# Kernel optimization log

Measured on AMD Instinct MI355X. Metric: run time of the kernel, lower is better.

## Reference

```python
import jax, jax.numpy as jnp
import numpy as np

H = 16  # number of heads

def setup_inputs() -> dict:
    key = jax.random.key(0)
    ks = jax.random.split(key, 8)
    B, T, D = 4, 2048, 1024
    s = 0.02
    return {
        "query": jax.random.normal(ks[0], (B, T, D), jnp.float32),
        "key":   jax.random.normal(ks[1], (B, T, D), jnp.float32),
        "value": jax.random.normal(ks[2], (B, T, D), jnp.float32),
        "mask":  jnp.ones((B, T, T), jnp.int32),
        # torch nn.Linear weights: [out_features, in_features]
        "Wq": jax.random.normal(ks[3], (D, D), jnp.float32) * s,
        "Wk": jax.random.normal(ks[4], (D, D), jnp.float32) * s,
        "Wv": jax.random.normal(ks[5], (D, D), jnp.float32) * s,
        "Wo": jax.random.normal(ks[6], (D, D), jnp.float32) * s,
        "bo": jnp.zeros((D,), jnp.float32),
    }

def reference(query, key, value, mask, Wq, Wk, Wv, Wo, bo):
    B, Tq, _ = query.shape
    Tk = key.shape[1]
    Dv = Wv.shape[0]
    # linear projections (y = x @ W^T), split into heads: [B, H, T, dh]
    Q = jnp.einsum('btd,ed->bte', query, Wq).reshape(B, Tq, H, -1).transpose(0, 2, 1, 3)
    K = jnp.einsum('btd,ed->bte', key,   Wk).reshape(B, Tk, H, -1).transpose(0, 2, 1, 3)
    V = jnp.einsum('btd,ed->bte', value, Wv).reshape(B, Tk, H, -1).transpose(0, 2, 1, 3)
    d_k = K.shape[-1]
    scores = jnp.einsum('bhqd,bhkd->bhqk', Q, K) / jnp.sqrt(jnp.asarray(d_k, Q.dtype))
    # mask broadcast: [B,1,Tq,Tk]; masked_fill(mask==0, -1e9)
    scores = jnp.where(mask[:, None] == 0, jnp.asarray(-1e9, scores.dtype), scores)
    attn = jax.nn.softmax(scores, axis=-1)
    Z = jnp.einsum('bhqk,bhkd->bhqd', attn, V)          # [B,H,Tq,dh]
    Zc = Z.transpose(0, 2, 1, 3).reshape(B, Tq, Dv)     # concat heads
    return jnp.einsum('btd,ed->bte', Zc, Wo) + bo
```

## Files before the change

kernel.cpp:

```cpp
#include <hip/hip_runtime.h>

typedef __bf16 bf16x8 __attribute__((ext_vector_type(8)));
typedef __bf16 bf16x4 __attribute__((ext_vector_type(4)));
typedef float f32x4 __attribute__((ext_vector_type(4)));
typedef unsigned short u16;
typedef unsigned long long u64;

#define NX 8388608
#define NW 1048576

__device__ __forceinline__ u16 f2bf(float f) {
  union { float f; unsigned u; } c; c.f = f;
  unsigned u = c.u;
  u += 0x7fffu + ((u >> 16) & 1u);
  return (u16)(u >> 16);
}

__device__ __forceinline__ f32x4 mfma16(bf16x8 a, bf16x8 b, f32x4 c) {
  return __builtin_amdgcn_mfma_f32_16x16x32_bf16(a, b, c, 0, 0, 0);
}

__device__ __forceinline__ void gld16(void* lds, const void* g) {
  __builtin_amdgcn_global_load_lds(
      (const __attribute__((address_space(1))) unsigned int*)g,
      (__attribute__((address_space(3))) unsigned int*)lds, 16, 0, 0);
}

__global__ __launch_bounds__(256) void cast_all(
    const float* __restrict__ q, const float* __restrict__ k,
    const float* __restrict__ v, const float* __restrict__ wq,
    const float* __restrict__ wk, const float* __restrict__ wv,
    const float* __restrict__ wo, u16* __restrict__ xbf, u16* __restrict__ wbf,
    const int* __restrict__ mask, u64* __restrict__ bits) {
  if (blockIdx.x >= 14336) {
    const int row = (blockIdx.x - 14336) * 4 + (threadIdx.x >> 6);
    const int lane = threadIdx.x & 63;
    const int* mrow = mask + (long long)row * 2048;
#pragma unroll
    for (int it = 0; it < 32; it++) {
      u64 w = __ballot(mrow[it * 64 + lane] != 0);
      if (lane == 0) bits[row * 32 + it] = w;
    }
    return;
  }
  long long i = ((long long)blockIdx.x * 256 + threadIdx.x) * 8;
  const float* src; u16* dst; long long off;
  if (i < (long long)NX)            { src = q; dst = xbf;            off = i; }
  else if (i < 2LL * NX)            { src = k; dst = xbf + NX;       off = i - NX; }
  else if (i < 3LL * NX)            { src = v; dst = xbf + 2LL * NX; off = i - 2LL * NX; }
  else {
    long long j = i - 3LL * NX;
    int w = (int)(j / NW); off = j - (long long)w * NW;
    src = (w == 0) ? wq : (w == 1) ? wk : (w == 2) ? wv : wo;
    dst = wbf + (long long)w * NW;
  }
  float4 a = *(const float4*)(src + off);
  float4 b = *(const float4*)(src + off + 4);
  u16 o[8] = {f2bf(a.x), f2bf(a.y), f2bf(a.z), f2bf(a.w),
              f2bf(b.x), f2bf(b.y), f2bf(b.z), f2bf(b.w)};
  *(uint4*)(dst + off) = *(const uint4*)o;
}

template <int MODE>
__global__ __launch_bounds__(256, 4) void gemm128(
    const u16* __restrict__ Abase, const u16* __restrict__ Wbase,
    u16* __restrict__ oq, u16* __restrict__ ok, u16* __restrict__ ovt,
    const float* __restrict__ bias, float* __restrict__ of) {
  __shared__ alignas(16) u16 smem[2][128 * 64];
  u16* sA = smem[0];
  u16* sB = smem[1];
  const u16* A = Abase;
  const u16* W = Wbase;
  if (MODE == 0) { A += (long long)blockIdx.z * NX; W += (long long)blockIdx.z * NW; }
  const int tid = threadIdx.x, wave = tid >> 6, lane = tid & 63;
  const int quad = lane >> 4, l15 = lane & 15;
  const int id = blockIdx.y * 8 + blockIdx.x;
  const int id2 = (id & 7) * 64 + (id >> 3);
  const int m0 = (id2 >> 3) * 128, n0 = (id2 & 7) * 128;
  const int wm = (wave & 1) * 64, wn = (wave >> 1) * 64;
  const int lr = lane >> 3;
  const int gc = (lane & 7) ^ lr;
  f32x4 acc[4][4];
#pragma unroll
  for (int i = 0; i < 4; i++)
#pragma unroll
    for (int j = 0; j < 4; j++) acc[i][j] = (f32x4){0.f, 0.f, 0.f, 0.f};

  for (int ks = 0; ks < 16; ks++) {
    const int k0 = ks * 64;
    __syncthreads();
#pragma unroll
    for (int t = 0; t < 4; t++) {
      const int rb = wave * 32 + t * 8;
      gld16(&sA[rb * 64], &A[(m0 + rb + lr) * 1024 + k0 + gc * 8]);
      gld16(&sB[rb * 64], &W[(n0 + rb + lr) * 1024 + k0 + gc * 8]);
    }
    __syncthreads();
#pragma unroll
    for (int kc = 0; kc < 2; kc++) {
      bf16x8 aF[4], bF[4];
#pragma unroll
      for (int i = 0; i < 4; i++)
        aF[i] = *(const bf16x8*)&sA[(wm + 16 * i + l15) * 64 +
                                    (((kc * 4 + quad) ^ (l15 & 7)) * 8)];
#pragma unroll
      for (int j = 0; j < 4; j++)
        bF[j] = *(const bf16x8*)&sB[(wn + 16 * j + l15) * 64 +
                                    (((kc * 4 + quad) ^ (l15 & 7)) * 8)];
#pragma unroll
      for (int i = 0; i < 4; i++)
#pragma unroll
        for (int j = 0; j < 4; j++) acc[i][j] = mfma16(aF[i], bF[j], acc[i][j]);
    }
  }

  if (MODE == 0) {
    const int z = blockIdx.z;
    __syncthreads();
    if (z < 2) {
      const float qscale = (z == 0) ? 0.18033688f : 1.0f;
      u16* dst = (z == 0) ? oq : ok;
      u16* sT = &smem[0][0] + wave * 4096;
#pragma unroll
      for (int i = 0; i < 4; i++)
#pragma unroll
        for (int j = 0; j < 4; j++)
#pragma unroll
          for (int r = 0; r < 4; r++) {
            int m = 16 * i + quad * 4 + r;
            int d = 16 * j + l15;
            sT[m * 64 + (((d >> 3) ^ (m & 7)) * 8) + (d & 7)] =
                f2bf(acc[i][j][r] * qscale);
          }
      const int bq = m0 >> 11, t0w = (m0 + wm) & 2047;
      const int hq = (n0 + wn) >> 6;
      u16* dq = dst + ((long long)((bq << 4) + hq) * 2048 + t0w + lane) * 64;
#pragma unroll
      for (int c = 0; c < 8; c++) {
        uint4 val = *(const uint4*)&sT[lane * 64 + ((c ^ (lane & 7)) * 8)];
        *(uint4*)(dq + c * 8) = val;
      }
    } else {
      u16* sT = &smem[0][0] + wave * 4096;
#pragma unroll
      for (int i = 0; i < 4; i++)
#pragma unroll
        for (int j = 0; j < 4; j++)
#pragma unroll
          for (int r = 0; r < 4; r++) {
            int m = 16 * i + quad * 4 + r;
            int n = 16 * j + l15;
            sT[n * 64 + (((m >> 3) ^ (n & 7)) * 8) + (m & 7)] = f2bf(acc[i][j][r]);
          }
      const int b = m0 >> 11, t0 = (m0 + wm) & 2047;
      const int h = (n0 + wn) >> 6;
      u16* dst = ovt + ((long long)((b << 4) + h)) * 131072 + lane * 2048 + t0;
#pragma unroll
      for (int c = 0; c < 8; c++) {
        uint4 val = *(const uint4*)&sT[lane * 64 + ((c ^ (lane & 7)) * 8)];
        *(uint4*)(dst + c * 8) = val;
      }
    }
  } else {
    float bb[4];
#pragma unroll
    for (int j = 0; j < 4; j++) bb[j] = bias[n0 + wn + 16 * j + l15];
    __syncthreads();
    float* sW = (float*)&smem[0][0] + wave * 2048;
#pragma unroll
    for (int p = 0; p < 2; p++) {
#pragma unroll
      for (int i = 0; i < 4; i++)
#pragma unroll
        for (int jj = 0; jj < 2; jj++)
#pragma unroll
          for (int r = 0; r < 4; r++) {
            int m = 16 * i + quad * 4 + r;
            int d = 16 * jj + l15;
            sW[m * 32 + (((d >> 2) ^ (m & 7)) * 4) + (d & 3)] =
                acc[i][2 * p + jj][r] + bb[2 * p + jj];
          }
      float* dof = of + (long long)(m0 + wm + lane) * 1024 + n0 + wn + p * 32;
#pragma unroll
      for (int c = 0; c < 8; c++) {
        float4 val = *(const float4*)&sW[lane * 32 + ((c ^ (lane & 7)) * 4)];
        *(float4*)(dof + c * 4) = val;
      }
    }
  }
}

__device__ __forceinline__ void stage_tile(
    u16* sKb, u16* sVb, const u16* __restrict__ Kh, const u16* __restrict__ Vt,
    int bh, int kt, int wave, int lr8, int gc8) {
#pragma unroll
  for (int t = 0; t < 2; t++) {
    const int rb = wave * 16 + t * 8;
    const int c = rb + lr8;
    const int kap = (c & 32) + (((c >> 2) & 3) << 3) + ((c & 16) >> 2) + (c & 3);
    gld16(&sKb[rb * 64], &Kh[(bh * 2048 + kt * 64 + kap) * 64 + gc8 * 8]);
    gld16(&sVb[rb * 64], &Vt[(bh * 64 + rb + lr8) * 2048 + kt * 64 + gc8 * 8]);
  }
}

__global__ __launch_bounds__(256, 4) void attn(
    const u16* __restrict__ Qh, const u16* __restrict__ Kh,
    const u16* __restrict__ Vt, const u64* __restrict__ mbits,
    u16* __restrict__ Zc) {
  __shared__ alignas(16) u16 sK[2][64 * 64];
  __shared__ alignas(16) u16 sV[2][64 * 64];
  const int tid = threadIdx.x, wave = tid >> 6, lane = tid & 63;
  const int quad = lane >> 4, l15 = lane & 15;
  const int id = blockIdx.y * 16 + blockIdx.x;
  const int id2 = (id & 7) * 128 + (id >> 3);
  const int bh = id2 >> 4, qt = id2 & 15;
  const int b = bh >> 4, h = bh & 15;
  const int q0 = qt * 128 + wave * 32;
  const int lr8 = lane >> 3, gc8 = (lane & 7) ^ lr8;

  bf16x8 qa[2][2];
#pragma unroll
  for (int g = 0; g < 2; g++)
#pragma unroll
    for (int kc = 0; kc < 2; kc++)
      qa[g][kc] = *(const bf16x8*)&Qh[(bh * 2048 + q0 + g * 16 + l15) * 64 +
                                      kc * 32 + quad * 8];

  const u64* mrow = mbits + (long long)(b * 2048 + q0) * 32;
  u64 am = ~0ull;
#pragma unroll
  for (int i = 0; i < 16; i++) am &= mrow[lane * 16 + i];
  const bool allfull = __all(am == ~0ull);

  f32x4 oacc[2][4];
#pragma unroll
  for (int g = 0; g < 2; g++)
#pragma unroll
    for (int j = 0; j < 4; j++) oacc[g][j] = (f32x4){0.f, 0.f, 0.f, 0.f};
  float lv[2] = {0.f, 0.f};

  stage_tile(&sK[0][0], &sV[0][0], Kh, Vt, bh, 0, wave, lr8, gc8);
  const f32x4 z4 = (f32x4){0.f, 0.f, 0.f, 0.f};

  for (int kt = 0; kt < 32; kt++) {
    const int cur = kt & 1;
    __syncthreads();
    if (kt < 31)
      stage_tile(&sK[cur ^ 1][0], &sV[cur ^ 1][0], Kh, Vt, bh, kt + 1,
                 wave, lr8, gc8);

    bf16x8 kF[2][4];
#pragma unroll
    for (int kc = 0; kc < 2; kc++)
#pragma unroll
      for (int j = 0; j < 4; j++)
        kF[kc][j] = *(const bf16x8*)&sK[cur][(16 * j + l15) * 64 +
                                            (((kc * 4 + quad) ^ (l15 & 7)) * 8)];
    f32x4 sacc[2][4];
    __builtin_amdgcn_s_setprio(1);
#pragma unroll
    for (int j = 0; j < 4; j++)
#pragma unroll
      for (int g = 0; g < 2; g++) sacc[g][j] = mfma16(kF[0][j], qa[g][0], z4);
#pragma unroll
    for (int j = 0; j < 4; j++)
#pragma unroll
      for (int g = 0; g < 2; g++)
        sacc[g][j] = mfma16(kF[1][j], qa[g][1], sacc[g][j]);
    __builtin_amdgcn_s_setprio(0);

    bf16x8 pa[2][2];
    if (allfull) {
#pragma unroll
      for (int g = 0; g < 2; g++) {
        float ls = 0.f;
#pragma unroll
        for (int kc = 0; kc < 2; kc++) {
          bf16x8 pk;
#pragma unroll
          for (int e = 0; e < 8; e++) {
            float p = __builtin_amdgcn_exp2f(sacc[g][2 * kc + (e >> 2)][e & 3]);
            ls += p;
            pk[e] = (__bf16)p;
          }
          pa[g][kc] = pk;
        }
        lv[g] += ls;
      }
    } else {
#pragma unroll
      for (int g = 0; g < 2; g++) {
        u64 w = mbits[(long long)(b * 2048 + q0 + g * 16 + l15) * 32 + kt];
        float ls = 0.f;
#pragma unroll
        for (int kc = 0; kc < 2; kc++) {
          bf16x8 pk;
#pragma unroll
          for (int e = 0; e < 8; e++) {
            float p = __builtin_amdgcn_exp2f(sacc[g][2 * kc + (e >> 2)][e & 3]);
            p = ((w >> (32 * kc + 8 * quad + e)) & 1ull) ? p : 0.f;
            ls += p;
            pk[e] = (__bf16)p;
          }
          pa[g][kc] = pk;
        }
        lv[g] += ls;
      }
    }

    bf16x8 vF[2][4];
#pragma unroll
    for (int kc = 0; kc < 2; kc++)
#pragma unroll
      for (int j = 0; j < 4; j++)
        vF[kc][j] = *(const bf16x8*)&sV[cur][(16 * j + l15) * 64 +
                                             (((kc * 4 + quad) ^ (l15 & 7)) * 8)];
    __builtin_amdgcn_s_setprio(1);
#pragma unroll
    for (int kc = 0; kc < 2; kc++)
#pragma unroll
      for (int g = 0; g < 2; g++)
#pragma unroll
        for (int j = 0; j < 4; j++)
          oacc[g][j] = mfma16(pa[g][kc], vF[kc][j], oacc[g][j]);
    __builtin_amdgcn_s_setprio(0);
  }

#pragma unroll
  for (int g = 0; g < 2; g++) {
    float s = lv[g];
    s += __shfl_xor(s, 16);
    s += __shfl_xor(s, 32);
    float inv[4];
#pragma unroll
    for (int r = 0; r < 4; r++)
      inv[r] = 1.f / __shfl(s, quad * 4 + r);
#pragma unroll
    for (int j = 0; j < 4; j++)
#pragma unroll
      for (int r = 0; r < 4; r++) {
        int t = q0 + g * 16 + quad * 4 + r;
        Zc[(b * 2048 + t) * 1024 + h * 64 + 16 * j + l15] =
            f2bf(oacc[g][j][r] * inv[r]);
      }
  }
}

extern "C" void kernel_launch(void* const* d_in, const int* in_sizes, int n_in,
                              void* d_out, int out_size, void* d_ws, size_t ws_size,
                              hipStream_t stream) {
  (void)in_sizes; (void)n_in; (void)out_size; (void)ws_size;
  const float* q    = (const float*)d_in[0];
  const float* k    = (const float*)d_in[1];
  const float* v    = (const float*)d_in[2];
  const int*   mask = (const int*)d_in[3];
  const float* Wq   = (const float*)d_in[4];
  const float* Wk   = (const float*)d_in[5];
  const float* Wv   = (const float*)d_in[6];
  const float* Wo   = (const float*)d_in[7];
  const float* bo   = (const float*)d_in[8];
  float* out = (float*)d_out;

  u16* Xbf = (u16*)d_ws;
  u16* Wbf = Xbf + 3LL * NX;
  u16* Qh  = Wbf + 4LL * NW;
  u16* Kh  = Qh + (long long)NX;
  u16* Vt  = Kh + (long long)NX;
  u16* Zc  = Vt + (long long)NX;
  u64* Mb  = (u64*)(Zc + (long long)NX);

  cast_all<<<16384, 256, 0, stream>>>(q, k, v, Wq, Wk, Wv, Wo, Xbf, Wbf, mask, Mb);
  gemm128<0><<<dim3(8, 64, 3), 256, 0, stream>>>(Xbf, Wbf, Qh, Kh, Vt, nullptr, nullptr);
  attn<<<dim3(16, 64), 256, 0, stream>>>(Qh, Kh, Vt, Mb, Zc);
  gemm128<1><<<dim3(8, 64), 256, 0, stream>>>(Zc, Wbf + 3LL * NW, nullptr, nullptr, nullptr,
                                              bo, out);
}
```

Measured before the change: 396.6 us.

## Double-buffer LDS tiles in projection GEMM to overlap global loads with MFMA

```diff
diff --git a/kernel.cpp b/kernel.cpp
--- a/kernel.cpp
+++ b/kernel.cpp
@@ -61,14 +61,23 @@
   *(uint4*)(dst + off) = *(const uint4*)o;
 }
 
+__device__ __forceinline__ void gstage(
+    u16* sAb, u16* sBb, const u16* __restrict__ A, const u16* __restrict__ W,
+    int m0, int n0, int k0, int wave, int lr, int gc) {
+#pragma unroll
+  for (int t = 0; t < 4; t++) {
+    const int rb = wave * 32 + t * 8;
+    gld16(&sAb[rb * 64], &A[(m0 + rb + lr) * 1024 + k0 + gc * 8]);
+    gld16(&sBb[rb * 64], &W[(n0 + rb + lr) * 1024 + k0 + gc * 8]);
+  }
+}
+
 template <int MODE>
-__global__ __launch_bounds__(256, 4) void gemm128(
+__global__ __launch_bounds__(256, 2) void gemm128(
     const u16* __restrict__ Abase, const u16* __restrict__ Wbase,
     u16* __restrict__ oq, u16* __restrict__ ok, u16* __restrict__ ovt,
     const float* __restrict__ bias, float* __restrict__ of) {
-  __shared__ alignas(16) u16 smem[2][128 * 64];
-  u16* sA = smem[0];
-  u16* sB = smem[1];
+  __shared__ alignas(16) u16 smem[2][2][128 * 64];
   const u16* A = Abase;
   const u16* W = Wbase;
   if (MODE == 0) { A += (long long)blockIdx.z * NX; W += (long long)blockIdx.z * NW; }
@@ -86,32 +95,39 @@
 #pragma unroll
     for (int j = 0; j < 4; j++) acc[i][j] = (f32x4){0.f, 0.f, 0.f, 0.f};
 
+  gstage(smem[0][0], smem[0][1], A, W, m0, n0, 0, wave, lr, gc);
+  int buf = 0;
   for (int ks = 0; ks < 16; ks++) {
-    const int k0 = ks * 64;
-    __syncthreads();
-#pragma unroll
-    for (int t = 0; t < 4; t++) {
-      const int rb = wave * 32 + t * 8;
-      gld16(&sA[rb * 64], &A[(m0 + rb + lr) * 1024 + k0 + gc * 8]);
-      gld16(&sB[rb * 64], &W[(n0 + rb + lr) * 1024 + k0 + gc * 8]);
-    }
-    __syncthreads();
+    if (ks < 15) {
+      gstage(smem[buf ^ 1][0], smem[buf ^ 1][1], A, W, m0, n0, (ks + 1) * 64,
+             wave, lr, gc);
+      asm volatile("s_waitcnt vmcnt(8)" ::: "memory");
+    } else {
+      asm volatile("s_waitcnt vmcnt(0)" ::: "memory");
+    }
+    __builtin_amdgcn_s_barrier();
+    __builtin_amdgcn_sched_barrier(0);
+    const u16* cA = smem[buf][0];
+    const u16* cB = smem[buf][1];
 #pragma unroll
     for (int kc = 0; kc < 2; kc++) {
       bf16x8 aF[4], bF[4];
 #pragma unroll
       for (int i = 0; i < 4; i++)
-        aF[i] = *(const bf16x8*)&sA[(wm + 16 * i + l15) * 64 +
+        aF[i] = *(const bf16x8*)&cA[(wm + 16 * i + l15) * 64 +
                                     (((kc * 4 + quad) ^ (l15 & 7)) * 8)];
 #pragma unroll
       for (int j = 0; j < 4; j++)
-        bF[j] = *(const bf16x8*)&sB[(wn + 16 * j + l15) * 64 +
+        bF[j] = *(const bf16x8*)&cB[(wn + 16 * j + l15) * 64 +
                                     (((kc * 4 + quad) ^ (l15 & 7)) * 8)];
 #pragma unroll
       for (int i = 0; i < 4; i++)
 #pragma unroll
         for (int j = 0; j < 4; j++) acc[i][j] = mfma16(aF[i], bF[j], acc[i][j]);
     }
+    __builtin_amdgcn_sched_barrier(0);
+    __builtin_amdgcn_s_barrier();
+    buf ^= 1;
   }
 
   if (MODE == 0) {
@@ -120,7 +136,7 @@
     if (z < 2) {
       const float qscale = (z == 0) ? 0.18033688f : 1.0f;
       u16* dst = (z == 0) ? oq : ok;
-      u16* sT = &smem[0][0] + wave * 4096;
+      u16* sT = &smem[0][0][0] + wave * 4096;
 #pragma unroll
       for (int i = 0; i < 4; i++)
 #pragma unroll
@@ -141,7 +157,7 @@
         *(uint4*)(dq + c * 8) = val;
       }
     } else {
-      u16* sT = &smem[0][0] + wave * 4096;
+      u16* sT = &smem[0][0][0] + wave * 4096;
 #pragma unroll
       for (int i = 0; i < 4; i++)
 #pragma unroll
@@ -166,7 +182,7 @@
 #pragma unroll
     for (int j = 0; j < 4; j++) bb[j] = bias[n0 + wn + 16 * j + l15];
     __syncthreads();
-    float* sW = (float*)&smem[0][0] + wave * 2048;
+    float* sW = (float*)&smem[0][0][0] + wave * 2048;
 #pragma unroll
     for (int p = 0; p < 2; p++) {
 #pragma unroll
```

Measured after the change: 390.1 us. Within noise of the previous version (-1.6%).
